# Optimization experiments

Hardware: AMD Instinct MI355X
Metric: run time of the kernel (lower is better)

## Reference

```python
import jax, jax.numpy as jnp
import numpy as np

QMIN, QMAX = 0.0, 255.0
# activation statistics (min, max) per layer, from init_kwargs['stats']
STATS = {"conv1": (-0.5, 3.0), "conv2": (0.0, 6.0), "fc1": (0.0, 8.0), "fc2": (0.0, 10.0)}


def calc_scale_zp(min_val, max_val):
    scale = (max_val - min_val) / (QMAX - QMIN)
    # original: int(clamped initial zero point) -> truncation
    zp = jnp.trunc(jnp.clip(QMIN - min_val / scale, QMIN, QMAX))
    return scale, zp


def quantize(x, min_val=None, max_val=None):
    if min_val is None:
        min_val, max_val = x.min(), x.max()
    scale, zp = calc_scale_zp(min_val, max_val)
    q = jnp.round(jnp.clip(zp + x / scale, QMIN, QMAX))
    return q, scale, zp


def conv2d(x, w, b):
    y = jax.lax.conv_general_dilated(x, w, (1, 1), "VALID",
                                     dimension_numbers=("NCHW", "OIHW", "NCHW"))
    return y + b[None, :, None, None]


def linear(x, w, b):
    return x @ w.T + b


def max_pool_2x2(x):
    return jax.lax.reduce_window(x, -jnp.inf, jax.lax.max, (1, 1, 2, 2), (1, 1, 2, 2), "VALID")


def quantize_layer(q_x, scale_x, zp_x, W, B, apply_fn, stat):
    # fake-quant weights/bias with their own min/max
    wq, scale_w, zp_w = quantize(W)
    bq, scale_b, zp_b = quantize(B)
    scale_next, zp_next = calc_scale_zp(stat[0], stat[1])
    X = q_x - zp_x
    W_eff = scale_x * scale_w * (wq - zp_w)
    B_eff = scale_b * (bq + zp_b)  # '+ zp_b' is faithful to the source
    y = jax.nn.relu(apply_fn(X, W_eff, B_eff) / scale_next + zp_next)
    # .round().byte() in torch wraps mod 256
    return jnp.mod(jnp.round(y), 256.0), scale_next, zp_next


def setup_inputs() -> dict:
    key = jax.random.key(0)
    ks = jax.random.split(key, 9)
    B = 4096
    return {
        "x": jax.random.normal(ks[0], (B, 1, 28, 28), jnp.float32),
        "conv1_w": jax.random.normal(ks[1], (20, 1, 5, 5), jnp.float32) * 0.1,
        "conv1_b": jax.random.normal(ks[2], (20,), jnp.float32) * 0.1,
        "conv2_w": jax.random.normal(ks[3], (50, 20, 5, 5), jnp.float32) * 0.05,
        "conv2_b": jax.random.normal(ks[4], (50,), jnp.float32) * 0.05,
        "fc1_w": jax.random.normal(ks[5], (500, 800), jnp.float32) * 0.03,
        "fc1_b": jax.random.normal(ks[6], (500,), jnp.float32) * 0.03,
        "fc2_w": jax.random.normal(ks[7], (10, 500), jnp.float32) * 0.05,
        "fc2_b": jax.random.normal(ks[8], (10,), jnp.float32) * 0.05,
    }


def reference(x, conv1_w, conv1_b, conv2_w, conv2_b, fc1_w, fc1_b, fc2_w, fc2_b):
    q, s, zp = quantize(x, STATS["conv1"][0], STATS["conv1"][1])
    q, s, zp = quantize_layer(q, s, zp, conv1_w, conv1_b, conv2d, STATS["conv2"])
    q = max_pool_2x2(q)                       # [B,20,12,12]
    q, s, zp = quantize_layer(q, s, zp, conv2_w, conv2_b, conv2d, STATS["fc1"])
    q = max_pool_2x2(q)                       # [B,50,4,4]
    q = q.reshape(-1, 4 * 4 * 50)             # [B,800]
    q, s, zp = quantize_layer(q, s, zp, fc1_w, fc1_b, linear, STATS["fc2"])
    xf = s * (q - zp)                         # dequantize
    logits = linear(xf, fc2_w, fc2_b)         # [B,10]
    return jax.nn.log_softmax(logits, axis=1)
```

## Files before the change

### kernel.cpp

```cpp
#include <hip/hip_runtime.h>
#include <cmath>

#define TPB 256
typedef float floatx4 __attribute__((ext_vector_type(4)));
typedef __bf16 bf16x8 __attribute__((ext_vector_type(8)));
typedef unsigned short ushort8 __attribute__((ext_vector_type(8)));
typedef unsigned int uintx4 __attribute__((ext_vector_type(4)));
typedef unsigned short ushort_t;

#define OFF_PMN 16
#define OFF_PMX 96
#define OFF_B1 520
#define OFF_B2 544
#define OFF_B3 600
#define W1BF_BYTE 6144
#define W2BF_BYTE 8192
#define W3BF_BYTE 131072
#define Q2_BYTE  29360128ULL

#define S_X1 (3.5f/255.0f)
#define ZP_X1 36.0f
#define S_N1 (6.0f/255.0f)
#define S_N2 (8.0f/255.0f)
#define S_N3 (10.0f/255.0f)

#define XSTR 40

__device__ const signed char TAPOF[32] = {
     0,  1,  2,  3,  4, -1,  5,  6,
     7,  8,  9, -1, 10, 11, 12, 13,
    14, -1, 15, 16, 17, 18, 19, -1,
    20, 21, 22, 23, 24, -1, -1, -1
};
__device__ const int OFFP[4][4] = {
    {0, 2, 4, 28},
    {30, 32, 56, 58},
    {60, 84, 86, 88},
    {112, 114, 116, 112}
};

__device__ inline float qclip(float x, float s, float zp){
    return rintf(fminf(fmaxf(zp + x / s, 0.0f), 255.0f));
}
__device__ inline ushort_t bfbits(float v){
    return (ushort_t)(__float_as_uint(v) >> 16);
}

__global__ __launch_bounds__(TPB) void k_minmax(
        const float* c1w, const float* c1b, const float* c2w, const float* c2b,
        const float* f1w, const float* f1b, float* pmn, float* pmx){
    __shared__ float smn[TPB], smx[TPB];
    int bb = blockIdx.x, tid = threadIdx.x;
    const float* src; int n, sub, nsub;
    if      (bb == 0){ src=c1w; n=500;    sub=0;     nsub=1;  }
    else if (bb == 1){ src=c1b; n=20;     sub=0;     nsub=1;  }
    else if (bb <  6){ src=c2w; n=25000;  sub=bb-2;  nsub=4;  }
    else if (bb == 6){ src=c2b; n=50;     sub=0;     nsub=1;  }
    else if (bb < 71){ src=f1w; n=400000; sub=bb-7;  nsub=64; }
    else             { src=f1b; n=500;    sub=0;     nsub=1;  }
    float mn = INFINITY, mx = -INFINITY;
    for (int i = sub*TPB + tid; i < n; i += nsub*TPB){
        float v = src[i]; mn = fminf(mn, v); mx = fmaxf(mx, v);
    }
    smn[tid] = mn; smx[tid] = mx; __syncthreads();
    for (int s = TPB/2; s > 0; s >>= 1){
        if (tid < s){
            smn[tid] = fminf(smn[tid], smn[tid+s]);
            smx[tid] = fmaxf(smx[tid], smx[tid+s]);
        }
        __syncthreads();
    }
    if (tid == 0){ pmn[bb] = smn[0]; pmx[bb] = smx[0]; }
}

#define N_EFF 452157
__global__ __launch_bounds__(TPB) void k_make_eff(
        const float* c1w, const float* c1b, const float* c2w, const float* c2b,
        const float* f1w, const float* f1b, const float* pmn, const float* pmx,
        float* ws, ushort_t* w1bf, ushort_t* w2bf, ushort_t* w3bf){
    __shared__ float sS[6], sZ[6];
    int tid = threadIdx.x;
    int wv = tid >> 6, lane = tid & 63;
    const int starts[6] = {0,1,2,6,7,71};
    const int counts[6] = {1,1,4,1,64,1};
    #pragma unroll
    for (int rep = 0; rep < 2; ++rep){
        int t = wv + rep*4;
        if (t < 6){
            float mn = INFINITY, mx = -INFINITY;
            if (lane < counts[t]){ mn = pmn[starts[t]+lane]; mx = pmx[starts[t]+lane]; }
            #pragma unroll
            for (int off = 32; off > 0; off >>= 1){
                mn = fminf(mn, __shfl_xor(mn, off));
                mx = fmaxf(mx, __shfl_xor(mx, off));
            }
            if (lane == 0){
                float s = (mx - mn) / 255.0f;
                sS[t] = s;
                sZ[t] = truncf(fminf(fmaxf(0.0f - mn / s, 0.0f), 255.0f));
            }
        }
    }
    __syncthreads();

    int i = blockIdx.x * TPB + tid;
    if (i >= N_EFF) return;
    if (i < 1024){
        int n = i >> 5, k = i & 31;
        int tap = (int)TAPOF[k];
        float v = 0.0f;
        if (n < 20 && tap >= 0) v = qclip(c1w[n*25 + tap], sS[0], sZ[0]) - sZ[0];
        w1bf[i] = bfbits(v);
    } else if (i < 1044){
        int j = i - 1024;
        ws[OFF_B1 + j] = (sS[1] * (qclip(c1b[j], sS[1], sZ[1]) + sZ[1])) / S_N1;
    } else if (i < 42004){
        int j = i - 1044;
        int c = j >> 11, r = j & 2047, co = r >> 5, k = r & 31;
        int q = k >> 3, jj = k & 7;
        int tap, ci; bool valid;
        if (c < 13){ tap = 2*c + (q>>1); ci = (q&1)*8 + jj; valid = (tap < 25); }
        else       { tap = 4*(c-13) + q; ci = 16 + jj;      valid = (tap < 25) && (jj < 4); }
        valid = valid && (co < 50);
        float v = 0.0f;
        if (valid) v = qclip(c2w[(co*20 + ci)*25 + tap], sS[2], sZ[2]) - sZ[2];
        w2bf[j] = bfbits(v);
    } else if (i < 42054){
        int j = i - 42004;
        ws[OFF_B2 + j] = (sS[3] * (qclip(c2b[j], sS[3], sZ[3]) + sZ[3])) / S_N2;
    } else if (i < 451654){
        int j = i - 42054;
        int n = j / 800, k = j - 800*n;
        float v = 0.0f;
        if (n < 500) v = qclip(f1w[n*800 + k], sS[4], sZ[4]) - sZ[4];
        w3bf[(((n>>4)*25 + (k>>5))*16 + (n&15))*32 + (k&31)] = bfbits(v);
    } else if (i < 452154){
        int j = i - 451654;
        ws[OFF_B3 + j] = (sS[5] * (qclip(f1b[j], sS[5], sZ[5]) + sZ[5])) / S_N3;
    } else if (i == 452154){
        ws[0] = (S_N1 * sS[2]) / S_N2;
    } else if (i == 452155){
        ws[1] = (S_N2 * sS[4]) / S_N3;
    } else {
        ws[2] = (S_X1 * sS[0]) / S_N1;
    }
}

__global__ __launch_bounds__(TPB, 4) void k_conv12(const float* x, const ushort_t* w1bf,
                                                   const ushort_t* w2bt, const float* ws,
                                                   ushort_t* q2bf, int B){
    __shared__ __align__(16) ushort_t xs[144*XSTR];
    __shared__ __align__(16) unsigned int ximp[784];
    int b = blockIdx.x, tid = threadIdx.x;
    int lane = tid & 63, wv = tid >> 6;
    int ln = lane & 15, quad = lane >> 4;

    for (int i = tid; i < 144; i += TPB){
        *(unsigned int*)(xs + i*XSTR + 20) = 0u;
        *(unsigned int*)(xs + i*XSTR + 22) = 0u;
    }

    const float* xb = x + (size_t)b * 784;
    if (tid < 196){
        floatx4 v = *(const floatx4*)(xb + tid*4);
        float x5 = (tid < 195) ? xb[tid*4 + 4] : 0.0f;
        ushort_t bq[5];
        #pragma unroll
        for (int j = 0; j < 4; ++j)
            bq[j] = bfbits(rintf(fminf(fmaxf(ZP_X1 + v[j] / S_X1, 0.0f), 255.0f)) - ZP_X1);
        bq[4] = bfbits(rintf(fminf(fmaxf(ZP_X1 + x5 / S_X1, 0.0f), 255.0f)) - ZP_X1);
        uintx4 P;
        #pragma unroll
        for (int j = 0; j < 4; ++j)
            P[j] = (unsigned int)bq[j] | ((unsigned int)bq[j+1] << 16);
        *(uintx4*)(ximp + tid*4) = P;
    }

    int o0 = OFFP[quad][0], o1 = OFFP[quad][1], o2 = OFFP[quad][2], o3 = OFFP[quad][3];

    ushort8 bw0 = *(const ushort8*)(w1bf + ln*32 + quad*8);
    ushort8 bw1 = *(const ushort8*)(w1bf + (16 + ln)*32 + quad*8);
    bf16x8 bf0 = __builtin_bit_cast(bf16x8, bw0);
    bf16x8 bf1 = __builtin_bit_cast(bf16x8, bw1);

    float K1 = ws[2];
    float B1_0 = ws[OFF_B1 + ln];
    float B1_1 = (ln < 4) ? ws[OFF_B1 + 16 + ln] : 0.0f;
    __syncthreads();

    #pragma unroll 3
    for (int i = 0; i < 9; ++i){
        int mt = 9*wv + i;
        int m = mt*16 + ln;
        int p = m >> 2, crn = m & 3;
        int ph_ = p / 12, pw_ = p - 12*ph_;
        int oh = 2*ph_ + (crn >> 1), ow = 2*pw_ + (crn & 1);
        int base = oh*28 + ow;
        uintx4 pv;
        pv[0] = ximp[base + o0];
        pv[1] = ximp[base + o1];
        pv[2] = ximp[base + o2];
        pv[3] = ximp[base + o3];
        bf16x8 af = __builtin_bit_cast(bf16x8, pv);
        floatx4 z = (floatx4){0.f,0.f,0.f,0.f};
        floatx4 a0 = __builtin_amdgcn_mfma_f32_16x16x32_bf16(af, bf0, z, 0, 0, 0);
        floatx4 a1 = __builtin_amdgcn_mfma_f32_16x16x32_bf16(af, bf1, z, 0, 0, 0);

        int pp = mt*4 + quad;
        {
            float y0 = fmaf(a0[0], K1, B1_0), y1 = fmaf(a0[1], K1, B1_0);
            float y2 = fmaf(a0[2], K1, B1_0), y3 = fmaf(a0[3], K1, B1_0);
            float mA = fmaxf(fmaxf(y0, y1), y2);
            float mf = fmaxf(fmaxf(mA, y3), 0.0f);
            if (__ballot(mf >= 255.5f)){
                unsigned int q0 = ((unsigned int)rintf(fmaxf(y0,0.f))) & 255u;
                unsigned int q1 = ((unsigned int)rintf(fmaxf(y1,0.f))) & 255u;
                unsigned int qq2 = ((unsigned int)rintf(fmaxf(y2,0.f))) & 255u;
                unsigned int q3 = ((unsigned int)rintf(fmaxf(y3,0.f))) & 255u;
                unsigned int h0 = q0 > q1 ? q0 : q1;
                unsigned int h1 = qq2 > q3 ? qq2 : q3;
                mf = (float)(h0 > h1 ? h0 : h1);
            } else {
                mf = rintf(mf);
            }
            xs[pp*XSTR + ln] = bfbits(mf);
        }
        if (ln < 4){
            float y0 = fmaf(a1[0], K1, B1_1), y1 = fmaf(a1[1], K1, B1_1);
            float y2 = fmaf(a1[2], K1, B1_1), y3 = fmaf(a1[3], K1, B1_1);
            float mA = fmaxf(fmaxf(y0, y1), y2);
            float mf = fmaxf(fmaxf(mA, y3), 0.0f);
            if (__ballot(mf >= 255.5f)){
                unsigned int q0 = ((unsigned int)rintf(fmaxf(y0,0.f))) & 255u;
                unsigned int q1 = ((unsigned int)rintf(fmaxf(y1,0.f))) & 255u;
                unsigned int qq2 = ((unsigned int)rintf(fmaxf(y2,0.f))) & 255u;
                unsigned int q3 = ((unsigned int)rintf(fmaxf(y3,0.f))) & 255u;
                unsigned int h0 = q0 > q1 ? q0 : q1;
                unsigned int h1 = qq2 > q3 ? qq2 : q3;
                mf = (float)(h0 > h1 ? h0 : h1);
            } else {
                mf = rintf(mf);
            }
            xs[pp*XSTR + 16 + ln] = bfbits(mf);
        }
    }
    __syncthreads();

    int mt0 = (wv & 1) * 2;
    int nt0 = (wv >> 1) * 2;
    int abase[2];
    #pragma unroll
    for (int mi = 0; mi < 2; ++mi)
        abase[mi] = (24*(mt0+mi) + (ln>>3)*12 + (ln&7)) * XSTR;
    int aoff[20];
    #pragma unroll
    for (int c = 0; c < 20; ++c){
        int tap, inner;
        if (c < 13){ tap = 2*c + (quad>>1); inner = (quad&1)*8; }
        else       { tap = 4*(c-13) + quad; inner = 16; }
        int pt = 0;
        if (tap < 25){ int kh = tap/5, kw = tap-5*kh; pt = kh*12 + kw; }
        aoff[c] = pt*XSTR + inner;
    }

    float sc2d = ws[0];
    const ushort_t* bsrc0 = w2bt + (size_t)(nt0*16 + ln)*32 + quad*8;
    const ushort_t* bsrc1 = bsrc0 + 16*32;

    floatx4 acc[2][2];
    #pragma unroll
    for (int mi = 0; mi < 2; ++mi)
        #pragma unroll
        for (int ni = 0; ni < 2; ++ni) acc[mi][ni] = (floatx4){0.f,0.f,0.f,0.f};

    #pragma unroll
    for (int c = 0; c < 20; ++c){
        ushort8 b0w = *(const ushort8*)(bsrc0 + c*2048);
        ushort8 b1w = *(const ushort8*)(bsrc1 + c*2048);
        ushort8 a0w = *(const ushort8*)(xs + abase[0] + aoff[c]);
        ushort8 a1w = *(const ushort8*)(xs + abase[1] + aoff[c]);
        bf16x8 a0 = __builtin_bit_cast(bf16x8, a0w);
        bf16x8 a1 = __builtin_bit_cast(bf16x8, a1w);
        bf16x8 b0 = __builtin_bit_cast(bf16x8, b0w);
        bf16x8 b1 = __builtin_bit_cast(bf16x8, b1w);
        acc[0][0] = __builtin_amdgcn_mfma_f32_16x16x32_bf16(a0, b0, acc[0][0], 0, 0, 0);
        acc[0][1] = __builtin_amdgcn_mfma_f32_16x16x32_bf16(a0, b1, acc[0][1], 0, 0, 0);
        acc[1][0] = __builtin_amdgcn_mfma_f32_16x16x32_bf16(a1, b0, acc[1][0], 0, 0, 0);
        acc[1][1] = __builtin_amdgcn_mfma_f32_16x16x32_bf16(a1, b1, acc[1][1], 0, 0, 0);
    }

    int bg = b >> 4, brow = b & 15;
    #pragma unroll
    for (int ni = 0; ni < 2; ++ni){
        int co = (nt0 + ni)*16 + ln;
        float bias2d = (co < 50) ? ws[OFF_B2 + co] : 0.0f;
        #pragma unroll
        for (int mi = 0; mi < 2; ++mi){
            int mt = mt0 + mi;
            float y0 = fmaf(acc[mi][ni][0], sc2d, bias2d);
            float y1 = fmaf(acc[mi][ni][1], sc2d, bias2d);
            float y2 = fmaf(acc[mi][ni][2], sc2d, bias2d);
            float y3 = fmaf(acc[mi][ni][3], sc2d, bias2d);
            float f0 = fmaxf(fmaxf(y0, y1), 0.0f);
            float f1 = fmaxf(fmaxf(y2, y3), 0.0f);
            float g0 = __shfl_xor(f0, 32);
            float g1 = __shfl_xor(f1, 32);
            float v0f = fmaxf(f0, g0), v1f = fmaxf(f1, g1);
            if (__ballot(fmaxf(v0f, v1f) >= 255.5f)){
                unsigned int q0 = ((unsigned int)rintf(fmaxf(y0,0.f))) & 255u;
                unsigned int q1 = ((unsigned int)rintf(fmaxf(y1,0.f))) & 255u;
                unsigned int qq2 = ((unsigned int)rintf(fmaxf(y2,0.f))) & 255u;
                unsigned int q3 = ((unsigned int)rintf(fmaxf(y3,0.f))) & 255u;
                unsigned int h0 = q0 > q1 ? q0 : q1;
                unsigned int h1 = qq2 > q3 ? qq2 : q3;
                unsigned int p0 = (unsigned int)__shfl_xor((int)h0, 32);
                unsigned int p1 = (unsigned int)__shfl_xor((int)h1, 32);
                v0f = (float)(h0 > p0 ? h0 : p0);
                v1f = (float)(h1 > p1 ? h1 : p1);
            } else {
                v0f = rintf(v0f); v1f = rintf(v1f);
            }
            if (quad < 2 && co < 50){
                int k0 = co*16 + mt*4 + quad*2;
                size_t off = ((size_t)bg*25 + (k0 >> 5))*512 + brow*32 + (k0 & 31);
                q2bf[off]     = bfbits(v0f);
                q2bf[off + 1] = bfbits(v1f);
            }
        }
    }
}

__global__ __launch_bounds__(512) void k_fc12(const ushort_t* q2t, const ushort_t* w3t,
                                              const float* ws, const float* w2,
                                              const float* b2, float* out, int B){
    __shared__ float red[8*16*10];
    int tid = threadIdx.x;
    int lane = tid & 63, wv = tid >> 6;
    int ln = lane & 15, quad = lane >> 4;
    int gi = blockIdx.x;
    int b0 = gi * 16;

    const ushort_t* asrc = q2t + (size_t)gi*25*512 + ln*32 + quad*8;
    const ushort_t* bsrc = w3t + (size_t)(wv*4)*25*512 + ln*32 + quad*8;

    floatx4 acc[4];
    #pragma unroll
    for (int t = 0; t < 4; ++t) acc[t] = (floatx4){0.f,0.f,0.f,0.f};

    ushort8 aw = *(const ushort8*)(asrc);
    ushort8 bw[4];
    #pragma unroll
    for (int t = 0; t < 4; ++t) bw[t] = *(const ushort8*)(bsrc + t*12800);

    #pragma unroll
    for (int c = 0; c < 25; ++c){
        ushort8 aN; ushort8 bN[4];
        if (c < 24){
            aN = *(const ushort8*)(asrc + (c+1)*512);
            #pragma unroll
            for (int t = 0; t < 4; ++t)
                bN[t] = *(const ushort8*)(bsrc + t*12800 + (c+1)*512);
        }
        #pragma unroll
        for (int t = 0; t < 4; ++t)
            acc[t] = __builtin_amdgcn_mfma_f32_16x16x32_bf16(
                         __builtin_bit_cast(bf16x8, aw), __builtin_bit_cast(bf16x8, bw[t]),
                         acc[t], 0, 0, 0);
        aw = aN;
        #pragma unroll
        for (int t = 0; t < 4; ++t) bw[t] = bN[t];
    }

    float sc3d = ws[1];
    float xf[4][4];
    #pragma unroll
    for (int t = 0; t < 4; ++t){
        int col = wv*64 + t*16 + ln;
        float bias = (col < 500) ? ws[OFF_B3 + col] : 0.0f;
        #pragma unroll
        for (int r = 0; r < 4; ++r){
            float y = fmaxf(fmaf(acc[t][r], sc3d, bias), 0.0f);
            unsigned int q = ((unsigned int)rintf(y)) & 255u;
            xf[r][t] = (col < 500) ? S_N3 * (float)q : 0.0f;
        }
    }

    #pragma unroll
    for (int c = 0; c < 10; ++c){
        float p[4] = {0.f, 0.f, 0.f, 0.f};
        #pragma unroll
        for (int t = 0; t < 4; ++t){
            int col = wv*64 + t*16 + ln;
            float w = (col < 500) ? w2[c*500 + col] : 0.0f;
            #pragma unroll
            for (int r = 0; r < 4; ++r) p[r] = fmaf(xf[r][t], w, p[r]);
        }
        #pragma unroll
        for (int m = 1; m <= 8; m <<= 1)
            #pragma unroll
            for (int r = 0; r < 4; ++r) p[r] += __shfl_xor(p[r], m);
        if (ln == 0){
            #pragma unroll
            for (int r = 0; r < 4; ++r)
                red[(wv*16 + quad*4 + r)*10 + c] = p[r];
        }
    }
    __syncthreads();

    if (tid < 16){
        int row = tid;
        float lg[10], mx = -INFINITY;
        #pragma unroll
        for (int c = 0; c < 10; ++c){
            float s = b2[c];
            #pragma unroll
            for (int w = 0; w < 8; ++w) s += red[(w*16 + row)*10 + c];
            lg[c] = s; mx = fmaxf(mx, s);
        }
        float sum = 0.0f;
        #pragma unroll
        for (int c = 0; c < 10; ++c) sum += expf(lg[c] - mx);
        float ls = logf(sum);
        #pragma unroll
        for (int c = 0; c < 10; ++c)
            out[(size_t)(b0 + row)*10 + c] = lg[c] - mx - ls;
    }
}

extern "C" void kernel_launch(void* const* d_in, const int* in_sizes, int n_in,
                              void* d_out, int out_size, void* d_ws, size_t ws_size,
                              hipStream_t stream){
    const float* x   = (const float*)d_in[0];
    const float* c1w = (const float*)d_in[1];
    const float* c1b = (const float*)d_in[2];
    const float* c2w = (const float*)d_in[3];
    const float* c2b = (const float*)d_in[4];
    const float* f1w = (const float*)d_in[5];
    const float* f1b = (const float*)d_in[6];
    const float* f2w = (const float*)d_in[7];
    const float* f2b = (const float*)d_in[8];
    int B = in_sizes[0] / 784;

    float* ws = (float*)d_ws;
    float* pmn = ws + OFF_PMN;
    float* pmx = ws + OFF_PMX;
    ushort_t* w1bf = (ushort_t*)((char*)d_ws + W1BF_BYTE);
    ushort_t* w2bf = (ushort_t*)((char*)d_ws + W2BF_BYTE);
    ushort_t* w3bf = (ushort_t*)((char*)d_ws + W3BF_BYTE);
    ushort_t* q2bf = (ushort_t*)((char*)d_ws + Q2_BYTE);
    float* out = (float*)d_out;

    k_minmax<<<72, TPB, 0, stream>>>(c1w, c1b, c2w, c2b, f1w, f1b, pmn, pmx);
    k_make_eff<<<(N_EFF + TPB - 1)/TPB, TPB, 0, stream>>>(c1w, c1b, c2w, c2b, f1w, f1b, pmn, pmx, ws, w1bf, w2bf, w3bf);
    k_conv12<<<B, TPB, 0, stream>>>(x, w1bf, w2bf, ws, q2bf, B);
    k_fc12<<<B/16, 512, 0, stream>>>(q2bf, w3bf, ws, f2w, f2b, out, B);
}
```

Baseline: 154.9 us.

## Process two images per conv block to reuse conv2 weight fragments

The fused conv1/conv2 kernel now handles two images per workgroup, doubling the shared-memory staging buffers and accumulator sets, and launches half as many blocks. Each conv2 weight fragment loaded from global memory is reused across both images, and per-block setup such as conv1 weight and bias loads is amortized. The cost is more registers and more LDS per block, which may reduce occupancy under the launch-bounds hint, plus fewer blocks in the grid.

```diff
diff --git a/kernel.cpp b/kernel.cpp
--- a/kernel.cpp
+++ b/kernel.cpp
@@ -149,31 +149,36 @@
 __global__ __launch_bounds__(TPB, 4) void k_conv12(const float* x, const ushort_t* w1bf,
                                                    const ushort_t* w2bt, const float* ws,
                                                    ushort_t* q2bf, int B){
-    __shared__ __align__(16) ushort_t xs[144*XSTR];
-    __shared__ __align__(16) unsigned int ximp[784];
-    int b = blockIdx.x, tid = threadIdx.x;
+    __shared__ __align__(16) ushort_t xs[2][144*XSTR];
+    __shared__ __align__(16) unsigned int ximp[2][784];
+    int b0 = blockIdx.x * 2, tid = threadIdx.x;
     int lane = tid & 63, wv = tid >> 6;
     int ln = lane & 15, quad = lane >> 4;
 
-    for (int i = tid; i < 144; i += TPB){
-        *(unsigned int*)(xs + i*XSTR + 20) = 0u;
-        *(unsigned int*)(xs + i*XSTR + 22) = 0u;
-    }
-
-    const float* xb = x + (size_t)b * 784;
-    if (tid < 196){
-        floatx4 v = *(const floatx4*)(xb + tid*4);
-        float x5 = (tid < 195) ? xb[tid*4 + 4] : 0.0f;
-        ushort_t bq[5];
-        #pragma unroll
-        for (int j = 0; j < 4; ++j)
-            bq[j] = bfbits(rintf(fminf(fmaxf(ZP_X1 + v[j] / S_X1, 0.0f), 255.0f)) - ZP_X1);
-        bq[4] = bfbits(rintf(fminf(fmaxf(ZP_X1 + x5 / S_X1, 0.0f), 255.0f)) - ZP_X1);
-        uintx4 P;
-        #pragma unroll
-        for (int j = 0; j < 4; ++j)
-            P[j] = (unsigned int)bq[j] | ((unsigned int)bq[j+1] << 16);
-        *(uintx4*)(ximp + tid*4) = P;
+    for (int i = tid; i < 288; i += TPB){
+        int img = i >= 144 ? 1 : 0;
+        int p = i - img*144;
+        *(unsigned int*)(xs[img] + p*XSTR + 20) = 0u;
+        *(unsigned int*)(xs[img] + p*XSTR + 22) = 0u;
+    }
+
+    #pragma unroll
+    for (int img = 0; img < 2; ++img){
+        const float* xb = x + (size_t)(b0 + img) * 784;
+        if (tid < 196){
+            floatx4 v = *(const floatx4*)(xb + tid*4);
+            float x5 = (tid < 195) ? xb[tid*4 + 4] : 0.0f;
+            ushort_t bq[5];
+            #pragma unroll
+            for (int j = 0; j < 4; ++j)
+                bq[j] = bfbits(rintf(fminf(fmaxf(ZP_X1 + v[j] / S_X1, 0.0f), 255.0f)) - ZP_X1);
+            bq[4] = bfbits(rintf(fminf(fmaxf(ZP_X1 + x5 / S_X1, 0.0f), 255.0f)) - ZP_X1);
+            uintx4 P;
+            #pragma unroll
+            for (int j = 0; j < 4; ++j)
+                P[j] = (unsigned int)bq[j] | ((unsigned int)bq[j+1] << 16);
+            *(uintx4*)(&ximp[img][tid*4]) = P;
+        }
     }
 
     int o0 = OFFP[quad][0], o1 = OFFP[quad][1], o2 = OFFP[quad][2], o3 = OFFP[quad][3];
@@ -188,7 +193,6 @@
     float B1_1 = (ln < 4) ? ws[OFF_B1 + 16 + ln] : 0.0f;
     __syncthreads();
 
-    #pragma unroll 3
     for (int i = 0; i < 9; ++i){
         int mt = 9*wv + i;
         int m = mt*16 + ln;
@@ -196,52 +200,60 @@
         int ph_ = p / 12, pw_ = p - 12*ph_;
         int oh = 2*ph_ + (crn >> 1), ow = 2*pw_ + (crn & 1);
         int base = oh*28 + ow;
-        uintx4 pv;
-        pv[0] = ximp[base + o0];
-        pv[1] = ximp[base + o1];
-        pv[2] = ximp[base + o2];
-        pv[3] = ximp[base + o3];
-        bf16x8 af = __builtin_bit_cast(bf16x8, pv);
+        int pp = mt*4 + quad;
+
         floatx4 z = (floatx4){0.f,0.f,0.f,0.f};
-        floatx4 a0 = __builtin_amdgcn_mfma_f32_16x16x32_bf16(af, bf0, z, 0, 0, 0);
-        floatx4 a1 = __builtin_amdgcn_mfma_f32_16x16x32_bf16(af, bf1, z, 0, 0, 0);
-
-        int pp = mt*4 + quad;
-        {
-            float y0 = fmaf(a0[0], K1, B1_0), y1 = fmaf(a0[1], K1, B1_0);
-            float y2 = fmaf(a0[2], K1, B1_0), y3 = fmaf(a0[3], K1, B1_0);
-            float mA = fmaxf(fmaxf(y0, y1), y2);
-            float mf = fmaxf(fmaxf(mA, y3), 0.0f);
-            if (__ballot(mf >= 255.5f)){
-                unsigned int q0 = ((unsigned int)rintf(fmaxf(y0,0.f))) & 255u;
-                unsigned int q1 = ((unsigned int)rintf(fmaxf(y1,0.f))) & 255u;
-                unsigned int qq2 = ((unsigned int)rintf(fmaxf(y2,0.f))) & 255u;
-                unsigned int q3 = ((unsigned int)rintf(fmaxf(y3,0.f))) & 255u;
-                unsigned int h0 = q0 > q1 ? q0 : q1;
-                unsigned int h1 = qq2 > q3 ? qq2 : q3;
-                mf = (float)(h0 > h1 ? h0 : h1);
-            } else {
-                mf = rintf(mf);
+        floatx4 a0i[2], a1i[2];
+        #pragma unroll
+        for (int img = 0; img < 2; ++img){
+            uintx4 pv;
+            pv[0] = ximp[img][base + o0];
+            pv[1] = ximp[img][base + o1];
+            pv[2] = ximp[img][base + o2];
+            pv[3] = ximp[img][base + o3];
+            bf16x8 af = __builtin_bit_cast(bf16x8, pv);
+            a0i[img] = __builtin_amdgcn_mfma_f32_16x16x32_bf16(af, bf0, z, 0, 0, 0);
+            a1i[img] = __builtin_amdgcn_mfma_f32_16x16x32_bf16(af, bf1, z, 0, 0, 0);
+        }
+
+        #pragma unroll
+        for (int img = 0; img < 2; ++img){
+            {
+                float y0 = fmaf(a0i[img][0], K1, B1_0), y1 = fmaf(a0i[img][1], K1, B1_0);
+                float y2 = fmaf(a0i[img][2], K1, B1_0), y3 = fmaf(a0i[img][3], K1, B1_0);
+                float mA = fmaxf(fmaxf(y0, y1), y2);
+                float mf = fmaxf(fmaxf(mA, y3), 0.0f);
+                if (__ballot(mf >= 255.5f)){
+                    unsigned int q0 = ((unsigned int)rintf(fmaxf(y0,0.f))) & 255u;
+                    unsigned int q1 = ((unsigned int)rintf(fmaxf(y1,0.f))) & 255u;
+                    unsigned int qq2 = ((unsigned int)rintf(fmaxf(y2,0.f))) & 255u;
+                    unsigned int q3 = ((unsigned int)rintf(fmaxf(y3,0.f))) & 255u;
+                    unsigned int h0 = q0 > q1 ? q0 : q1;
+                    unsigned int h1 = qq2 > q3 ? qq2 : q3;
+                    mf = (float)(h0 > h1 ? h0 : h1);
+                } else {
+                    mf = rintf(mf);
+                }
+                xs[img][pp*XSTR + ln] = bfbits(mf);
             }
-            xs[pp*XSTR + ln] = bfbits(mf);
-        }
-        if (ln < 4){
-            float y0 = fmaf(a1[0], K1, B1_1), y1 = fmaf(a1[1], K1, B1_1);
-            float y2 = fmaf(a1[2], K1, B1_1), y3 = fmaf(a1[3], K1, B1_1);
-            float mA = fmaxf(fmaxf(y0, y1), y2);
-            float mf = fmaxf(fmaxf(mA, y3), 0.0f);
-            if (__ballot(mf >= 255.5f)){
-                unsigned int q0 = ((unsigned int)rintf(fmaxf(y0,0.f))) & 255u;
-                unsigned int q1 = ((unsigned int)rintf(fmaxf(y1,0.f))) & 255u;
-                unsigned int qq2 = ((unsigned int)rintf(fmaxf(y2,0.f))) & 255u;
-                unsigned int q3 = ((unsigned int)rintf(fmaxf(y3,0.f))) & 255u;
-                unsigned int h0 = q0 > q1 ? q0 : q1;
-                unsigned int h1 = qq2 > q3 ? qq2 : q3;
-                mf = (float)(h0 > h1 ? h0 : h1);
-            } else {
-                mf = rintf(mf);
+            if (ln < 4){
+                float y0 = fmaf(a1i[img][0], K1, B1_1), y1 = fmaf(a1i[img][1], K1, B1_1);
+                float y2 = fmaf(a1i[img][2], K1, B1_1), y3 = fmaf(a1i[img][3], K1, B1_1);
+                float mA = fmaxf(fmaxf(y0, y1), y2);
+                float mf = fmaxf(fmaxf(mA, y3), 0.0f);
+                if (__ballot(mf >= 255.5f)){
+                    unsigned int q0 = ((unsigned int)rintf(fmaxf(y0,0.f))) & 255u;
+                    unsigned int q1 = ((unsigned int)rintf(fmaxf(y1,0.f))) & 255u;
+                    unsigned int qq2 = ((unsigned int)rintf(fmaxf(y2,0.f))) & 255u;
+                    unsigned int q3 = ((unsigned int)rintf(fmaxf(y3,0.f))) & 255u;
+                    unsigned int h0 = q0 > q1 ? q0 : q1;
+                    unsigned int h1 = qq2 > q3 ? qq2 : q3;
+                    mf = (float)(h0 > h1 ? h0 : h1);
+                } else {
+                    mf = rintf(mf);
+                }
+                xs[img][pp*XSTR + 16 + ln] = bfbits(mf);
             }
-            xs[pp*XSTR + 16 + ln] = bfbits(mf);
         }
     }
     __syncthreads();
@@ -267,64 +279,73 @@
     const ushort_t* bsrc0 = w2bt + (size_t)(nt0*16 + ln)*32 + quad*8;
     const ushort_t* bsrc1 = bsrc0 + 16*32;
 
-    floatx4 acc[2][2];
-    #pragma unroll
-    for (int mi = 0; mi < 2; ++mi)
-        #pragma unroll
-        for (int ni = 0; ni < 2; ++ni) acc[mi][ni] = (floatx4){0.f,0.f,0.f,0.f};
+    floatx4 acc[2][2][2];
+    #pragma unroll
+    for (int g = 0; g < 2; ++g)
+        #pragma unroll
+        for (int mi = 0; mi < 2; ++mi)
+            #pragma unroll
+            for (int ni = 0; ni < 2; ++ni) acc[g][mi][ni] = (floatx4){0.f,0.f,0.f,0.f};
 
     #pragma unroll
     for (int c = 0; c < 20; ++c){
         ushort8 b0w = *(const ushort8*)(bsrc0 + c*2048);
         ushort8 b1w = *(const ushort8*)(bsrc1 + c*2048);
-        ushort8 a0w = *(const ushort8*)(xs + abase[0] + aoff[c]);
-        ushort8 a1w = *(const ushort8*)(xs + abase[1] + aoff[c]);
-        bf16x8 a0 = __builtin_bit_cast(bf16x8, a0w);
-        bf16x8 a1 = __builtin_bit_cast(bf16x8, a1w);
-        bf16x8 b0 = __builtin_bit_cast(bf16x8, b0w);
-        bf16x8 b1 = __builtin_bit_cast(bf16x8, b1w);
-        acc[0][0] = __builtin_amdgcn_mfma_f32_16x16x32_bf16(a0, b0, acc[0][0], 0, 0, 0);
-        acc[0][1] = __builtin_amdgcn_mfma_f32_16x16x32_bf16(a0, b1, acc[0][1], 0, 0, 0);
-        acc[1][0] = __builtin_amdgcn_mfma_f32_16x16x32_bf16(a1, b0, acc[1][0], 0, 0, 0);
-        acc[1][1] = __builtin_amdgcn_mfma_f32_16x16x32_bf16(a1, b1, acc[1][1], 0, 0, 0);
-    }
-
-    int bg = b >> 4, brow = b & 15;
-    #pragma unroll
-    for (int ni = 0; ni < 2; ++ni){
-        int co = (nt0 + ni)*16 + ln;
-        float bias2d = (co < 50) ? ws[OFF_B2 + co] : 0.0f;
-        #pragma unroll
-        for (int mi = 0; mi < 2; ++mi){
-            int mt = mt0 + mi;
-            float y0 = fmaf(acc[mi][ni][0], sc2d, bias2d);
-            float y1 = fmaf(acc[mi][ni][1], sc2d, bias2d);
-            float y2 = fmaf(acc[mi][ni][2], sc2d, bias2d);
-            float y3 = fmaf(acc[mi][ni][3], sc2d, bias2d);
-            float f0 = fmaxf(fmaxf(y0, y1), 0.0f);
-            float f1 = fmaxf(fmaxf(y2, y3), 0.0f);
-            float g0 = __shfl_xor(f0, 32);
-            float g1 = __shfl_xor(f1, 32);
-            float v0f = fmaxf(f0, g0), v1f = fmaxf(f1, g1);
-            if (__ballot(fmaxf(v0f, v1f) >= 255.5f)){
-                unsigned int q0 = ((unsigned int)rintf(fmaxf(y0,0.f))) & 255u;
-                unsigned int q1 = ((unsigned int)rintf(fmaxf(y1,0.f))) & 255u;
-                unsigned int qq2 = ((unsigned int)rintf(fmaxf(y2,0.f))) & 255u;
-                unsigned int q3 = ((unsigned int)rintf(fmaxf(y3,0.f))) & 255u;
-                unsigned int h0 = q0 > q1 ? q0 : q1;
-                unsigned int h1 = qq2 > q3 ? qq2 : q3;
-                unsigned int p0 = (unsigned int)__shfl_xor((int)h0, 32);
-                unsigned int p1 = (unsigned int)__shfl_xor((int)h1, 32);
-                v0f = (float)(h0 > p0 ? h0 : p0);
-                v1f = (float)(h1 > p1 ? h1 : p1);
-            } else {
-                v0f = rintf(v0f); v1f = rintf(v1f);
-            }
-            if (quad < 2 && co < 50){
-                int k0 = co*16 + mt*4 + quad*2;
-                size_t off = ((size_t)bg*25 + (k0 >> 5))*512 + brow*32 + (k0 & 31);
-                q2bf[off]     = bfbits(v0f);
-                q2bf[off + 1] = bfbits(v1f);
+        bf16x8 bb0 = __builtin_bit_cast(bf16x8, b0w);
+        bf16x8 bb1 = __builtin_bit_cast(bf16x8, b1w);
+        #pragma unroll
+        for (int img = 0; img < 2; ++img){
+            ushort8 a0w = *(const ushort8*)(xs[img] + abase[0] + aoff[c]);
+            ushort8 a1w = *(const ushort8*)(xs[img] + abase[1] + aoff[c]);
+            bf16x8 a0 = __builtin_bit_cast(bf16x8, a0w);
+            bf16x8 a1 = __builtin_bit_cast(bf16x8, a1w);
+            acc[img][0][0] = __builtin_amdgcn_mfma_f32_16x16x32_bf16(a0, bb0, acc[img][0][0], 0, 0, 0);
+            acc[img][0][1] = __builtin_amdgcn_mfma_f32_16x16x32_bf16(a0, bb1, acc[img][0][1], 0, 0, 0);
+            acc[img][1][0] = __builtin_amdgcn_mfma_f32_16x16x32_bf16(a1, bb0, acc[img][1][0], 0, 0, 0);
+            acc[img][1][1] = __builtin_amdgcn_mfma_f32_16x16x32_bf16(a1, bb1, acc[img][1][1], 0, 0, 0);
+        }
+    }
+
+    #pragma unroll
+    for (int img = 0; img < 2; ++img){
+        int b = b0 + img;
+        int bg = b >> 4, brow = b & 15;
+        #pragma unroll
+        for (int ni = 0; ni < 2; ++ni){
+            int co = (nt0 + ni)*16 + ln;
+            float bias2d = (co < 50) ? ws[OFF_B2 + co] : 0.0f;
+            #pragma unroll
+            for (int mi = 0; mi < 2; ++mi){
+                int mt = mt0 + mi;
+                float y0 = fmaf(acc[img][mi][ni][0], sc2d, bias2d);
+                float y1 = fmaf(acc[img][mi][ni][1], sc2d, bias2d);
+                float y2 = fmaf(acc[img][mi][ni][2], sc2d, bias2d);
+                float y3 = fmaf(acc[img][mi][ni][3], sc2d, bias2d);
+                float f0 = fmaxf(fmaxf(y0, y1), 0.0f);
+                float f1 = fmaxf(fmaxf(y2, y3), 0.0f);
+                float g0 = __shfl_xor(f0, 32);
+                float g1 = __shfl_xor(f1, 32);
+                float v0f = fmaxf(f0, g0), v1f = fmaxf(f1, g1);
+                if (__ballot(fmaxf(v0f, v1f) >= 255.5f)){
+                    unsigned int q0 = ((unsigned int)rintf(fmaxf(y0,0.f))) & 255u;
+                    unsigned int q1 = ((unsigned int)rintf(fmaxf(y1,0.f))) & 255u;
+                    unsigned int qq2 = ((unsigned int)rintf(fmaxf(y2,0.f))) & 255u;
+                    unsigned int q3 = ((unsigned int)rintf(fmaxf(y3,0.f))) & 255u;
+                    unsigned int h0 = q0 > q1 ? q0 : q1;
+                    unsigned int h1 = qq2 > q3 ? qq2 : q3;
+                    unsigned int p0 = (unsigned int)__shfl_xor((int)h0, 32);
+                    unsigned int p1 = (unsigned int)__shfl_xor((int)h1, 32);
+                    v0f = (float)(h0 > p0 ? h0 : p0);
+                    v1f = (float)(h1 > p1 ? h1 : p1);
+                } else {
+                    v0f = rintf(v0f); v1f = rintf(v1f);
+                }
+                if (quad < 2 && co < 50){
+                    int k0 = co*16 + mt*4 + quad*2;
+                    size_t off = ((size_t)bg*25 + (k0 >> 5))*512 + brow*32 + (k0 & 31);
+                    q2bf[off]     = bfbits(v0f);
+                    q2bf[off + 1] = bfbits(v1f);
+                }
             }
         }
     }
@@ -452,6 +473,6 @@
 
     k_minmax<<<72, TPB, 0, stream>>>(c1w, c1b, c2w, c2b, f1w, f1b, pmn, pmx);
     k_make_eff<<<(N_EFF + TPB - 1)/TPB, TPB, 0, stream>>>(c1w, c1b, c2w, c2b, f1w, f1b, pmn, pmx, ws, w1bf, w2bf, w3bf);
-    k_conv12<<<B, TPB, 0, stream>>>(x, w1bf, w2bf, ws, q2bf, B);
+    k_conv12<<<B/2, TPB, 0, stream>>>(x, w1bf, w2bf, ws, q2bf, B);
     k_fc12<<<B/16, 512, 0, stream>>>(q2bf, w3bf, ws, f2w, f2b, out, B);
 }
```

Measured after the change: 143.3 us, median of 2. -7.5%, faster.
